# Kernel optimization log

Hardware: AMD Instinct MI355X
Metric: run time of the kernel (lower is better)

The kernel has to match this reference:

```python
import jax, jax.numpy as jnp
import numpy as np

N_NODES = 4096
IN_FEATURES = 256
N_HEADS = 8
N_HIDDEN = 32  # out_features // n_heads = 256 // 8
NEG_SLOPE = 0.2
MASK_FILL = -1e9


def setup_inputs() -> dict:
    key = jax.random.key(0)
    k_h, k_adj, k_w, k_a = jax.random.split(key, 4)
    h = jax.random.normal(k_h, (N_NODES, IN_FEATURES), dtype=jnp.float32)
    adj_mat = jax.random.randint(k_adj, (N_NODES, N_NODES, 1), 0, 2, dtype=jnp.int32)
    # linear: Linear(in_features, n_hidden*n_heads, bias=False) -> W: [in, H*F]
    W = jax.random.normal(k_w, (IN_FEATURES, N_HEADS * N_HIDDEN), dtype=jnp.float32) / np.sqrt(IN_FEATURES)
    # attn: Linear(2*n_hidden, 1, bias=False) -> a: [2*F]
    a = jax.random.normal(k_a, (2 * N_HIDDEN,), dtype=jnp.float32) / np.sqrt(2 * N_HIDDEN)
    return {"h": h, "adj_mat": adj_mat, "W": W, "a": a}


def reference(h, adj_mat, W, a):
    n = h.shape[0]
    # g: [n, H, F]
    g = (h @ W).reshape(n, N_HEADS, N_HIDDEN)
    # attn(concat(g_i, g_j)) == g_i . a[:F] + g_j . a[F:]  (decomposed, same math,
    # avoids materializing the O(N^2 * H * 2F) concat tensor of the torch code)
    a_src, a_dst = a[:N_HIDDEN], a[N_HIDDEN:]
    s_src = jnp.einsum('nhf,f->nh', g, a_src)  # [n, H]
    s_dst = jnp.einsum('nhf,f->nh', g, a_dst)  # [n, H]
    e = jax.nn.leaky_relu(s_src[:, None, :] + s_dst[None, :, :], negative_slope=NEG_SLOPE)  # [n, n, H]
    e = jnp.where(adj_mat == 0, MASK_FILL, e)  # adj_mat [n, n, 1] broadcasts over heads
    att = jax.nn.softmax(e, axis=1)  # softmax over source nodes j (dropout in eval mode = identity)
    out = jnp.einsum('ijh,jhf->ihf', att, g)  # [n, H, F]
    return out.reshape(n, N_HEADS * N_HIDDEN)  # is_concat=True
```

## Files before the change

kernel.cpp:

```cpp
#include <hip/hip_runtime.h>

#define NN 4096
#define FIN 256
#define CC 256
#define NH 8
#define NW32 (NN / 32)

typedef __attribute__((ext_vector_type(8))) short short8;
typedef __attribute__((ext_vector_type(4))) float f32x4;
typedef __attribute__((ext_vector_type(4))) unsigned int u32x4;

__device__ __forceinline__ unsigned cvtpk_bf16(float lo, float hi) {
  unsigned r;
  asm("v_cvt_pk_bf16_f32 %0, %1, %2" : "=v"(r) : "v"(lo), "v"(hi));
  return r;
}

__device__ __forceinline__ unsigned short bf16rn(float x) {
  unsigned int u = __builtin_bit_cast(unsigned int, x);
  u += 0x7fffu + ((u >> 16) & 1u);
  return (unsigned short)(u >> 16);
}

__device__ __forceinline__ void gl_lds16(const void* g, void* l) {
  __builtin_amdgcn_global_load_lds(
      (const __attribute__((address_space(1))) void*)g,
      (__attribute__((address_space(3))) void*)l, 16, 0, 0);
}

#define GROWS 8
#define GEMM_BLKS (NN / GROWS)
#define BP_BLKS (NN * NW32 / 256)
__global__ __launch_bounds__(256) void k_gemm(
    const float* __restrict__ h, const float* __restrict__ W,
    const float* __restrict__ a, const int* __restrict__ adj,
    unsigned int* __restrict__ adjb, unsigned short* __restrict__ gTs,
    float4* __restrict__ spack, float* __restrict__ dtc) {
  __shared__ float hs[GROWS][FIN];
  const int t = threadIdx.x;
  const int bx = blockIdx.x;

  if (bx >= GEMM_BLKS) {
    const int wid = (bx - GEMM_BLKS) * 256 + t;
    const int row = wid >> 7, wd = wid & 127;
    const int* src = adj + (size_t)row * NN + wd * 32;
    int4 v[8];
#pragma unroll
    for (int s = 0; s < 8; ++s) v[s] = *(const int4*)&src[s * 4];
    unsigned int bits = 0;
#pragma unroll
    for (int s = 0; s < 8; ++s) {
      bits |= (v[s].x ? 1u : 0u) << (s * 4 + 0);
      bits |= (v[s].y ? 1u : 0u) << (s * 4 + 1);
      bits |= (v[s].z ? 1u : 0u) << (s * 4 + 2);
      bits |= (v[s].w ? 1u : 0u) << (s * 4 + 3);
    }
    adjb[(size_t)row * NW32 + wd] = bits;
    return;
  }

  const int r0 = bx * GROWS;
#pragma unroll
  for (int idx = t; idx < GROWS * FIN / 4; idx += 256) {
    const int r = idx >> 6, c4 = idx & 63;
    *(float4*)&hs[r][c4 * 4] =
        *(const float4*)&h[(size_t)(r0 + r) * FIN + c4 * 4];
  }
  __syncthreads();
  const int c = t;
  float acc[GROWS];
#pragma unroll
  for (int r = 0; r < GROWS; ++r) acc[r] = 0.f;
  for (int k = 0; k < FIN; k += 4) {
    const float w0 = W[(size_t)(k + 0) * CC + c];
    const float w1 = W[(size_t)(k + 1) * CC + c];
    const float w2 = W[(size_t)(k + 2) * CC + c];
    const float w3 = W[(size_t)(k + 3) * CC + c];
#pragma unroll
    for (int r = 0; r < GROWS; ++r) {
      const float4 hv = *(const float4*)&hs[r][k];
      acc[r] += hv.x * w0 + hv.y * w1 + hv.z * w2 + hv.w * w3;
    }
  }
  const int f = c & 31, hh = c >> 5;
  const float aS = a[f], aD = a[32 + f];
  unsigned short gu[GROWS];
#pragma unroll
  for (int r = 0; r < GROWS; ++r) {
    float ps = acc[r] * aS, pd = acc[r] * aD;
#pragma unroll
    for (int m = 1; m < 32; m <<= 1) {
      ps += __shfl_xor(ps, m, 64);
      pd += __shfl_xor(pd, m, 64);
    }
    if (f == 0) {
      const int n = r0 + r;
      spack[(size_t)hh * NN + n] =
          make_float4(__expf(ps), __expf(0.2f * ps), 0.f, 0.f);
      float* dc = dtc + ((size_t)hh * (NN / 32) + (n >> 5)) * 64 + (n & 31);
      dc[0] = __expf(pd);
      dc[32] = __expf(0.2f * pd);
    }
    gu[r] = bf16rn(acc[r]);
  }
  uint4 gv;
  gv.x = (unsigned)gu[0] | ((unsigned)gu[1] << 16);
  gv.y = (unsigned)gu[2] | ((unsigned)gu[3] << 16);
  gv.z = (unsigned)gu[4] | ((unsigned)gu[5] << 16);
  gv.w = (unsigned)gu[6] | ((unsigned)gu[7] << 16);
  const int jc = r0 >> 5, qq = (r0 >> 3) & 3;
  const int p = qq ^ ((c >> 1) & 3);
  *(uint4*)(gTs + ((size_t)jc * 1024 + c * 4 + p) * 8) = gv;
}

__global__ __launch_bounds__(256, 3) void k_attn(
    const unsigned int* __restrict__ adjb, const unsigned short* __restrict__ gTs,
    const float4* __restrict__ spack, const float* __restrict__ dtc,
    float* __restrict__ out) {
  __shared__ unsigned short gt_lds[4][2][2048];
  auto red = (float(*)[2][3][4][64]) & gt_lds[0][0][0];

  const int lane = threadIdx.x & 63;
  const int w = threadIdx.x >> 6;
  const int il = lane & 15, q = lane >> 4;
  const int bx = blockIdx.x;
  const int hh = bx & 7;
  const int ib = bx >> 3;
  const int i0 = ib * 32;

  float e1v[2], e2v[2];
#pragma unroll
  for (int it = 0; it < 2; ++it) {
    const float4 v = spack[(size_t)hh * NN + i0 + it * 16 + il];
    e1v[it] = v.x; e2v[it] = v.y;
  }

  f32x4 acc[2][2];
  f32x4 lac[2];
#pragma unroll
  for (int it = 0; it < 2; ++it) {
#pragma unroll
    for (int r = 0; r < 4; ++r) lac[it][r] = 0.f;
#pragma unroll
    for (int ft = 0; ft < 2; ++ft)
#pragma unroll
      for (int r = 0; r < 4; ++r) acc[it][ft][r] = 0.f;
  }

  const short8 ones = {(short)0x3F80, (short)0x3F80, (short)0x3F80,
                       (short)0x3F80, (short)0x3F80, (short)0x3F80,
                       (short)0x3F80, (short)0x3F80};

  const unsigned long long* abr0 =
      (const unsigned long long*)(adjb + (size_t)(i0 + il) * NW32) + w * 16;
  const unsigned long long* abr1 =
      (const unsigned long long*)(adjb + (size_t)(i0 + 16 + il) * NW32) +
      w * 16;
  const float* dbase = dtc + ((size_t)hh * (NN / 32) + w * 32) * 64;
  const int sh = q * 8;
  const int u0 = il * 4 + (q ^ ((il >> 1) & 3));

  auto stage = [&](int buf, int rr) {
    const unsigned short* src =
        gTs + (((size_t)(w * 32 + rr * 2)) * 1024 + hh * 128) * 8;
    char* dst = (char*)&gt_lds[w][buf][0];
    gl_lds16(src + (size_t)lane * 8, dst);
    gl_lds16(src + (size_t)(64 + lane) * 8, dst + 1024);
    gl_lds16(src + (size_t)(1024 + lane) * 8, dst + 2048);
    gl_lds16(src + (size_t)(1024 + 64 + lane) * 8, dst + 3072);
  };

  unsigned long long Ab0, Ab1, Bb0, Bb1;
  float4 Ad0, Ad1, Ad2, Ad3, Ad4, Ad5, Ad6, Ad7;
  float4 Bd0, Bd1, Bd2, Bd3, Bd4, Bd5, Bd6, Bd7;

#define ISSUE_REGS(P, rr)                                  \
  {                                                        \
    P##b0 = abr0[rr]; P##b1 = abr1[rr];                    \
    const float* dp_ = dbase + (size_t)(rr) * 128;         \
    P##d0 = *(const float4*)(dp_ + q * 8);                 \
    P##d1 = *(const float4*)(dp_ + q * 8 + 4);             \
    P##d2 = *(const float4*)(dp_ + 32 + q * 8);            \
    P##d3 = *(const float4*)(dp_ + 32 + q * 8 + 4);        \
    P##d4 = *(const float4*)(dp_ + 64 + q * 8);            \
    P##d5 = *(const float4*)(dp_ + 64 + q * 8 + 4);        \
    P##d6 = *(const float4*)(dp_ + 96 + q * 8);            \
    P##d7 = *(const float4*)(dp_ + 96 + q * 8 + 4);        \
  }

#define COMPUTE(P)                                                          \
  {                                                                         \
    _Pragma("unroll") for (int sub = 0; sub < 2; ++sub) {                   \
      const unsigned int bits0 = (unsigned int)(P##b0 >> (sub * 32));       \
      const unsigned int bits1 = (unsigned int)(P##b1 >> (sub * 32));       \
      float e1j[8], e2j[8];                                                 \
      if (sub == 0) {                                                       \
        *(float4*)&e1j[0] = P##d0; *(float4*)&e1j[4] = P##d1;               \
        *(float4*)&e2j[0] = P##d2; *(float4*)&e2j[4] = P##d3;               \
      } else {                                                              \
        *(float4*)&e1j[0] = P##d4; *(float4*)&e1j[4] = P##d5;               \
        *(float4*)&e2j[0] = P##d6; *(float4*)&e2j[4] = P##d7;               \
      }                                                                     \
      const unsigned short* gb = &gt_lds[w][cur][sub * 1024];               \
      const short8 b0 = *(const short8*)&gb[u0 * 8];                        \
      const short8 b1 = *(const short8*)&gb[(u0 + 64) * 8];                 \
      _Pragma("unroll") for (int it = 0; it < 2; ++it) {                    \
        const unsigned int bits = it ? bits1 : bits0;                       \
        const float ei1 = e1v[it], ei2 = e2v[it];                           \
        float wv[8];                                                        \
        _Pragma("unroll") for (int e = 0; e < 8; ++e)                       \
            wv[e] = ((bits >> (sh + e)) & 1u)                               \
                        ? fmaxf(ei1 * e1j[e], ei2 * e2j[e])                 \
                        : 0.f;                                              \
        u32x4 uu;                                                           \
        _Pragma("unroll") for (int m = 0; m < 4; ++m)                       \
            uu[m] = cvtpk_bf16(wv[2 * m], wv[2 * m + 1]);                   \
        const short8 afr = __builtin_bit_cast(short8, uu);                  \
        acc[it][0] = __builtin_amdgcn_mfma_f32_16x16x32_bf16(               \
            afr, b0, acc[it][0], 0, 0, 0);                                  \
        acc[it][1] = __builtin_amdgcn_mfma_f32_16x16x32_bf16(               \
            afr, b1, acc[it][1], 0, 0, 0);                                  \
        lac[it] = __builtin_amdgcn_mfma_f32_16x16x32_bf16(                  \
            afr, ones, lac[it], 0, 0, 0);                                   \
      }                                                                     \
    }                                                                       \
  }

  stage(0, 0);
  ISSUE_REGS(A, 0);
  __syncthreads();
  int cur = 0;

#pragma unroll 1
  for (int r2 = 0; r2 < 8; ++r2) {
    const int r = r2 * 2;
    if (r + 1 < 16) { stage(cur ^ 1, r + 1); ISSUE_REGS(B, r + 1); }
    COMPUTE(A);
    __syncthreads();
    cur ^= 1;
    if (r + 2 < 16) { stage(cur ^ 1, r + 2); ISSUE_REGS(A, r + 2); }
    COMPUTE(B);
    __syncthreads();
    cur ^= 1;
  }
#undef ISSUE_REGS
#undef COMPUTE

  if (w >= 2) {
    const int s = w - 2;
#pragma unroll
    for (int it = 0; it < 2; ++it)
#pragma unroll
      for (int r = 0; r < 4; ++r) {
        red[s][it][0][r][lane] = acc[it][0][r];
        red[s][it][1][r][lane] = acc[it][1][r];
        red[s][it][2][r][lane] = lac[it][r];
      }
  }
  __syncthreads();
  if (w < 2) {
#pragma unroll
    for (int it = 0; it < 2; ++it)
#pragma unroll
      for (int r = 0; r < 4; ++r) {
        acc[it][0][r] += red[w][it][0][r][lane];
        acc[it][1][r] += red[w][it][1][r][lane];
        lac[it][r] += red[w][it][2][r][lane];
      }
  }
  __syncthreads();
  if (w == 1) {
#pragma unroll
    for (int it = 0; it < 2; ++it)
#pragma unroll
      for (int r = 0; r < 4; ++r) {
        red[0][it][0][r][lane] = acc[it][0][r];
        red[0][it][1][r][lane] = acc[it][1][r];
        red[0][it][2][r][lane] = lac[it][r];
      }
  }
  __syncthreads();
  if (w == 0) {
#pragma unroll
    for (int it = 0; it < 2; ++it)
#pragma unroll
      for (int r = 0; r < 4; ++r) {
        const float a0 = acc[it][0][r] + red[0][it][0][r][lane];
        const float a1 = acc[it][1][r] + red[0][it][1][r][lane];
        const float lsum = lac[it][r] + red[0][it][2][r][lane];
        const float inv = 1.f / lsum;
        const size_t irow = i0 + it * 16 + q * 4 + r;
        out[irow * CC + hh * 32 + il] = a0 * inv;
        out[irow * CC + hh * 32 + 16 + il] = a1 * inv;
      }
  }
}

extern "C" void kernel_launch(void* const* d_in, const int* in_sizes, int n_in,
                              void* d_out, int out_size, void* d_ws,
                              size_t ws_size, hipStream_t stream) {
  (void)in_sizes; (void)n_in; (void)out_size; (void)ws_size;
  const float* h = (const float*)d_in[0];
  const int* adj = (const int*)d_in[1];
  const float* W = (const float*)d_in[2];
  const float* a = (const float*)d_in[3];
  float* out = (float*)d_out;
  char* ws = (char*)d_ws;

  unsigned short* gTs = (unsigned short*)ws;
  float4* spack = (float4*)(ws + (size_t)NN * CC * 2);
  float* dtc = (float*)(spack + (size_t)NH * NN);
  unsigned int* adjb =
      (unsigned int*)(dtc + (size_t)NH * (NN / 32) * 64);

  k_gemm<<<GEMM_BLKS + BP_BLKS, 256, 0, stream>>>(h, W, a, adj, adjb, gTs,
                                                  spack, dtc);
  k_attn<<<(NN / 32) * NH, 256, 0, stream>>>(adjb, gTs, spack, dtc, out);
}
```

Baseline: 76.66 us.

## Replace per-stage barriers with vmcnt waits and two-deep prefetch pipeline

Restructures the main loop so both buffers are prefetched up front. Each compute step is guarded by an explicit s_waitcnt vmcnt instead of a __syncthreads after every stage, with a fixed buffer index per half. This removes workgroup barriers from the inner loop and keeps two stages of global loads in flight. It relies on LDS staging being per-wave (gt_lds indexed by w) and on the count of outstanding loads matching exactly 14, which is fragile if the compiler reorders or adds memory ops.

```diff
diff --git a/kernel.cpp b/kernel.cpp
--- a/kernel.cpp
+++ b/kernel.cpp
@@ -188,7 +188,10 @@
     P##d7 = *(const float4*)(dp_ + 96 + q * 8 + 4);        \
   }
 
-#define COMPUTE(P)                                                          \
+#define WAIT14 asm volatile("s_waitcnt vmcnt(14)" ::: "memory")
+#define WAIT0 asm volatile("s_waitcnt vmcnt(0)" ::: "memory")
+
+#define COMPUTE(P, BUF)                                                     \
   {                                                                         \
     _Pragma("unroll") for (int sub = 0; sub < 2; ++sub) {                   \
       const unsigned int bits0 = (unsigned int)(P##b0 >> (sub * 32));       \
@@ -201,7 +204,7 @@
         *(float4*)&e1j[0] = P##d4; *(float4*)&e1j[4] = P##d5;               \
         *(float4*)&e2j[0] = P##d6; *(float4*)&e2j[4] = P##d7;               \
       }                                                                     \
-      const unsigned short* gb = &gt_lds[w][cur][sub * 1024];               \
+      const unsigned short* gb = &gt_lds[w][BUF][sub * 1024];               \
       const short8 b0 = *(const short8*)&gb[u0 * 8];                        \
       const short8 b1 = *(const short8*)&gb[(u0 + 64) * 8];                 \
       _Pragma("unroll") for (int it = 0; it < 2; ++it) {                    \
@@ -228,23 +231,31 @@
 
   stage(0, 0);
   ISSUE_REGS(A, 0);
-  __syncthreads();
-  int cur = 0;
+  stage(1, 1);
+  ISSUE_REGS(B, 1);
 
 #pragma unroll 1
-  for (int r2 = 0; r2 < 8; ++r2) {
+  for (int r2 = 0; r2 < 7; ++r2) {
     const int r = r2 * 2;
-    if (r + 1 < 16) { stage(cur ^ 1, r + 1); ISSUE_REGS(B, r + 1); }
-    COMPUTE(A);
-    __syncthreads();
-    cur ^= 1;
-    if (r + 2 < 16) { stage(cur ^ 1, r + 2); ISSUE_REGS(A, r + 2); }
-    COMPUTE(B);
-    __syncthreads();
-    cur ^= 1;
-  }
+    WAIT14;
+    COMPUTE(A, 0);
+    stage(0, r + 2);
+    ISSUE_REGS(A, r + 2);
+    WAIT14;
+    COMPUTE(B, 1);
+    stage(1, r + 3);
+    ISSUE_REGS(B, r + 3);
+  }
+  WAIT14;
+  COMPUTE(A, 0);
+  WAIT0;
+  COMPUTE(B, 1);
 #undef ISSUE_REGS
 #undef COMPUTE
+#undef WAIT14
+#undef WAIT0
+
+  __syncthreads();
 
   if (w >= 2) {
     const int s = w - 2;
```

New measurement: 192.6 us. +151.2%, slower.
